# Kernel tuning notes

Hardware: AMD Instinct MI355X
Metric: run time of the kernel (lower is better)

Reference implementation:

```python
import jax, jax.numpy as jnp
import numpy as np

POINT_DIM, VOXEL_DIM, NUM_HEADS = 3, 256, 8
HEAD_DIM = VOXEL_DIM // NUM_HEADS


def _linear_params(key, fan_in, fan_out):
    kw, kb = jax.random.split(key)
    bound = 1.0 / np.sqrt(fan_in)
    W = jax.random.uniform(kw, (fan_out, fan_in), jnp.float32, -bound, bound)
    b = jax.random.uniform(kb, (fan_out,), jnp.float32, -bound, bound)
    return W, b


def setup_inputs() -> dict:
    key = jax.random.key(0)
    ks = jax.random.split(key, 7)
    points = jax.random.normal(ks[0], (2, 4096, POINT_DIM), jnp.float32)
    voxel_features = jax.random.normal(ks[1], (2, 2048, VOXEL_DIM), jnp.float32)
    Wp, bp = _linear_params(ks[2], POINT_DIM, VOXEL_DIM)
    Wq, bq = _linear_params(ks[3], VOXEL_DIM, VOXEL_DIM)
    Wk, bk = _linear_params(ks[4], VOXEL_DIM, VOXEL_DIM)
    Wv, bv = _linear_params(ks[5], VOXEL_DIM, VOXEL_DIM)
    Wf, bf = _linear_params(ks[6], VOXEL_DIM * 2, VOXEL_DIM)
    return {
        "points": points, "voxel_features": voxel_features,
        "Wp": Wp, "bp": bp, "Wq": Wq, "bq": bq,
        "Wk": Wk, "bk": bk, "Wv": Wv, "bv": bv,
        "Wf": Wf, "bf": bf,
    }


def reference(points, voxel_features, Wp, bp, Wq, bq, Wk, bk, Wv, bv, Wf, bf):
    B, N, _ = points.shape
    M = voxel_features.shape[1]
    # projections (torch Linear: x @ W.T + b)
    point_features = points @ Wp.T + bp                      # [B,N,D]
    q = (point_features @ Wq.T + bq).reshape(B, N, NUM_HEADS, HEAD_DIM)
    k = (voxel_features @ Wk.T + bk).reshape(B, M, NUM_HEADS, HEAD_DIM)
    v = (voxel_features @ Wv.T + bv).reshape(B, M, NUM_HEADS, HEAD_DIM)
    # attention scores [B,H,N,M]
    scale = 1.0 / np.sqrt(HEAD_DIM).astype(np.float32)
    attn = jnp.einsum('bnhd,bmhd->bhnm', q, k) * scale
    attn = jax.nn.softmax(attn, axis=-1)
    attended = jnp.einsum('bhnm,bmhd->bnhd', attn, v).reshape(B, N, VOXEL_DIM)
    fused = jnp.concatenate([point_features, attended], axis=-1) @ Wf.T + bf
    return fused
```

## Files before the change

### kernel.cpp

```cpp
#include <hip/hip_runtime.h>

#define B_ 2
#define N_ 4096
#define M_ 2048
#define D_ 256
#define H_ 8
#define DH_ 32
#define ROWS_ (B_*N_)
#define KVROWS_ (B_*M_)
#define PRE_ (0.17677669529663687f * 1.4426950408889634f)
#define CBASE_ 32.0f

typedef __attribute__((ext_vector_type(8))) short short8_t;
typedef __attribute__((ext_vector_type(4))) float float4_t;

#if defined(__has_builtin)
# if __has_builtin(__builtin_amdgcn_exp2f)
#  define EXP2F(x) __builtin_amdgcn_exp2f(x)
# else
#  define EXP2F(x) exp2f(x)
# endif
#else
# define EXP2F(x) exp2f(x)
#endif

__device__ __forceinline__ unsigned int rne_u(float f) {
    union { float f; unsigned int u; } c;
    c.f = f;
    return c.u + 0x7FFFu + ((c.u >> 16) & 1u);
}

__device__ __forceinline__ unsigned short f2us(float f) {
    return (unsigned short)(rne_u(f) >> 16);
}

__device__ __forceinline__ unsigned int pack2rn(float a, float b) {
    return __builtin_amdgcn_perm(rne_u(b), rne_u(a), 0x07060302u);
}

__device__ __forceinline__ unsigned int pack2tr(float a, float b) {
    union { float f; unsigned int u; } x, y;
    x.f = a; y.f = b;
    return __builtin_amdgcn_perm(y.u, x.u, 0x07060302u);
}

__device__ __forceinline__ short8_t cvt8(float4 a, float4 b) {
    union { unsigned int u[4]; short8_t s; } c;
    c.u[0] = pack2rn(a.x, a.y);
    c.u[1] = pack2rn(a.z, a.w);
    c.u[2] = pack2rn(b.x, b.y);
    c.u[3] = pack2rn(b.z, b.w);
    return c.s;
}

__device__ __forceinline__ int xcd_swz(int bid, int nwg) {
    const int cpx = nwg >> 3;
    return (bid & 7) * cpx + (bid >> 3);
}

template<int K, int NCOL, int LDSRC>
__device__ __forceinline__ void stageB2(const float* __restrict__ W, int col0, int kof,
                                        unsigned short* __restrict__ Bs, int tid)
{
    const int n = tid & (NCOL - 1), g = tid / NCOL;
    const int GROUPS = 256 / NCOL;
    const int CPT = (K / 8) / GROUPS;
    const float* src = W + (size_t)(col0 + n) * LDSRC + kof + g * (K / GROUPS);
#pragma unroll
    for (int ci = 0; ci < CPT; ci++) {
        int logc = g * CPT + ci;
        int phys = logc ^ (n & 7);
        short8_t v = cvt8(*(const float4*)(src + ci * 8), *(const float4*)(src + ci * 8 + 4));
        *(short8_t*)(Bs + (size_t)n * K + phys * 8) = v;
    }
}

template<int K>
__device__ __forceinline__ short8_t readB(const unsigned short* __restrict__ Bs,
                                          int c, int l16, int quad, int k0)
{
    int phys = ((k0 >> 3) + quad) ^ (l16 & 7);
    return *(const short8_t*)(Bs + (size_t)(16 * c + l16) * K + phys * 8);
}

__global__ __launch_bounds__(256) void g_projkv4(
    const float* __restrict__ voxel,
    const float* __restrict__ Wp, const float* __restrict__ bp,
    const float* __restrict__ Wq, const float* __restrict__ bq,
    const float* __restrict__ Wk, const float* __restrict__ bk,
    const float* __restrict__ Wv, const float* __restrict__ bv,
    const float* __restrict__ Wf, const float* __restrict__ bfb,
    unsigned short* __restrict__ k_g, unsigned short* __restrict__ vt_g,
    float* __restrict__ Wqc, float* __restrict__ Wfc)
{
    const int tid = threadIdx.x;
    const int wave = tid >> 6, lane = tid & 63, quad = lane >> 4, l16 = lane & 15;

    __shared__ unsigned short Bs[64 * 256];

    const int bid = (int)blockIdx.x;
    if (bid < 512) {
        const int lbid = xcd_swz(bid, 512);
        const int row0 = (lbid >> 3) * 64;
        const int sub  = lbid & 7;
        const int col0 = (sub >> 1) * 64;
        const bool isV = sub & 1;

        stageB2<256, 64, 256>(isV ? Wv : Wk, col0, 0, Bs, tid);

        const float* arow = voxel + (size_t)(row0 + wave * 16 + l16) * D_;
        short8_t af[8];
#pragma unroll
        for (int i = 0; i < 8; i++)
            af[i] = cvt8(*(const float4*)(arow + i * 32 + quad * 8),
                         *(const float4*)(arow + i * 32 + quad * 8 + 4));

        float4_t acc[4];
#pragma unroll
        for (int c = 0; c < 4; c++) acc[c] = (float4_t){0.f, 0.f, 0.f, 0.f};
        __syncthreads();
#pragma unroll
        for (int i = 0; i < 8; i++)
#pragma unroll
            for (int c = 0; c < 4; c++)
                acc[c] = __builtin_amdgcn_mfma_f32_16x16x32_bf16(af[i], readB<256>(Bs, c, l16, quad, i * 32), acc[c], 0, 0, 0);

        if (!isV) {
#pragma unroll
            for (int c = 0; c < 4; c++) {
                int col = col0 + 16 * c + l16;
                float bbk = bk[col];
#pragma unroll
                for (int r = 0; r < 4; r++) {
                    int row = row0 + wave * 16 + quad * 4 + r;
                    k_g[(size_t)row * D_ + col] = f2us(acc[c][r] + bbk);
                }
            }
        } else {
            const int b = row0 / M_;
            const int m0 = row0 - b * M_ + wave * 16 + quad * 4;
#pragma unroll
            for (int c = 0; c < 4; c++) {
                int col = col0 + 16 * c + l16;
                float bbv = bv[col];
                int h = col >> 5, dh = col & 31;
                unsigned int u0 = pack2rn(acc[c][0] + bbv, acc[c][1] + bbv);
                unsigned int u1 = pack2rn(acc[c][2] + bbv, acc[c][3] + bbv);
                *(uint2*)(vt_g + (size_t)((b * H_ + h) * DH_ + dh) * M_ + m0) = make_uint2(u0, u1);
            }
        }
    } else {
        const int role = bid - 512;
        float* wps = (float*)Bs;
        *(float4*)(wps + tid * 4) = make_float4(Wp[tid * 3 + 0], Wp[tid * 3 + 1],
                                                Wp[tid * 3 + 2], bp[tid]);
        __syncthreads();
        const int col = tid;
        const float* wrow = role ? (Wf + (size_t)col * 512) : (Wq + (size_t)col * 256);
        float a0 = 0.f, a1 = 0.f, a2 = 0.f, ab = 0.f;
#pragma unroll 4
        for (int d = 0; d < 256; d += 4) {
            float4 wv = *(const float4*)(wrow + d);
            float4 w0 = *(const float4*)(wps + (d + 0) * 4);
            float4 w1 = *(const float4*)(wps + (d + 1) * 4);
            float4 w2 = *(const float4*)(wps + (d + 2) * 4);
            float4 w3 = *(const float4*)(wps + (d + 3) * 4);
            a0 += wv.x * w0.x + wv.y * w1.x + wv.z * w2.x + wv.w * w3.x;
            a1 += wv.x * w0.y + wv.y * w1.y + wv.z * w2.y + wv.w * w3.y;
            a2 += wv.x * w0.z + wv.y * w1.z + wv.z * w2.z + wv.w * w3.z;
            ab += wv.x * w0.w + wv.y * w1.w + wv.z * w2.w + wv.w * w3.w;
        }
        if (role == 0) {
            *(float4*)(Wqc + (size_t)col * 4) =
                make_float4(a0 * PRE_, a1 * PRE_, a2 * PRE_, (ab + bq[col]) * PRE_);
        } else {
            *(float4*)(Wfc + (size_t)col * 4) =
                make_float4(a0, a1, a2, ab + bfb[col]);
        }
    }
}

__global__ __launch_bounds__(512) void k_attn10(
    const float* __restrict__ points, const float* __restrict__ Wqc,
    const unsigned short* __restrict__ k_g,
    const unsigned short* __restrict__ vt_g,
    unsigned short* __restrict__ att_g)
{
    const int tid = threadIdx.x;
    const int w = tid >> 6, lane = tid & 63, quad = lane >> 4, l16 = lane & 15;
    const int lbid = xcd_swz((int)blockIdx.x, B_ * H_ * (N_ / 128));
    const int nt = lbid & 31;
    const int bh = lbid >> 5;
    const int b = bh >> 3, h = bh & 7;
    const int n0 = nt * 128 + w * 16;

    __shared__ unsigned short Kt[2][64][40];
    __shared__ unsigned short Vt[2][32][72];

    const unsigned short* kbase = k_g + (size_t)(b * M_) * D_ + h * DH_;
    const unsigned short* vbase = vt_g + (size_t)(bh * DH_) * M_;

    const bool isK = (tid < 256);
    const int kr = tid >> 2, kc = tid & 3;
    const int vr = (tid - 256) >> 3, vc = tid & 7;
    const int ksr = kr ^ ((kr & 8) >> 1);

    const unsigned short* gq = isK ? (kbase + (size_t)kr * D_ + kc * 8)
                                   : (vbase + (size_t)vr * M_ + vc * 8);
    const int gstep = isK ? 64 * D_ : 64;
    unsigned short* ldst = isK ? (&Kt[0][0][0] + ksr * 40 + kc * 8)
                               : (&Vt[0][0][0] + vr * 72 + vc * 8);
    const int lstride = isK ? 2560 : 2304;

    *(short8_t*)ldst = *(const short8_t*)gq;

    const int rbas = 8 * (l16 >> 2) + (l16 & 3);
    const int rx = l16 & 4;
    int krow[4];
#pragma unroll
    for (int t = 0; t < 4; t++)
        krow[t] = (rbas + 4 * (t & 1) + 32 * (t >> 1)) ^ rx;

    const size_t qrow = (size_t)(b * N_ + n0 + l16);
    const float p0 = points[qrow * 3 + 0];
    const float p1 = points[qrow * 3 + 1];
    const float p2 = points[qrow * 3 + 2];
    float q8[8];
#pragma unroll
    for (int j = 0; j < 8; j++) {
        float4 wc = *(const float4*)(Wqc + (size_t)(h * DH_ + quad * 8 + j) * 4);
        q8[j] = p0 * wc.x + p1 * wc.y + p2 * wc.z + wc.w;
    }
    short8_t qf = cvt8(make_float4(q8[0], q8[1], q8[2], q8[3]),
                       make_float4(q8[4], q8[5], q8[6], q8[7]));

    float4_t od0 = {0.f, 0.f, 0.f, 0.f};
    float4_t od1 = {0.f, 0.f, 0.f, 0.f};
    float l_lane = 0.f;

    const float4_t zc = {-CBASE_, -CBASE_, -CBASE_, -CBASE_};

#pragma unroll 2
    for (int s = 0; s < M_ / 64; s++) {
        __syncthreads();
        const int buf = s & 1;
        const bool more = (s + 1 < M_ / 64);
        short8_t nxt;
        if (more) {
            gq += gstep;
            nxt = *(const short8_t*)gq;
        }

        float4_t st[4];
#pragma unroll
        for (int t = 0; t < 4; t++) {
            short8_t kf = *(const short8_t*)&Kt[buf][krow[t]][quad * 8];
            st[t] = __builtin_amdgcn_mfma_f32_16x16x32_bf16(kf, qf, zc, 0, 0, 0);
        }

        float psum = 0.f;
        unsigned int uu[4][2];
#pragma unroll
        for (int t = 0; t < 4; t++) {
            float p0e = EXP2F(st[t][0]);
            float p1e = EXP2F(st[t][1]);
            float p2e = EXP2F(st[t][2]);
            float p3e = EXP2F(st[t][3]);
            psum += (p0e + p1e) + (p2e + p3e);
            uu[t][0] = pack2tr(p0e, p1e);
            uu[t][1] = pack2tr(p2e, p3e);
        }
        l_lane += psum;

        union { unsigned int u[4]; short8_t s; } pa, pb2;
        pa.u[0]  = uu[0][0]; pa.u[1]  = uu[0][1]; pa.u[2]  = uu[1][0]; pa.u[3]  = uu[1][1];
        pb2.u[0] = uu[2][0]; pb2.u[1] = uu[2][1]; pb2.u[2] = uu[3][0]; pb2.u[3] = uu[3][1];

        short8_t vf00 = *(const short8_t*)&Vt[buf][l16][quad * 8];
        short8_t vf01 = *(const short8_t*)&Vt[buf][l16][32 + quad * 8];
        short8_t vf10 = *(const short8_t*)&Vt[buf][16 + l16][quad * 8];
        short8_t vf11 = *(const short8_t*)&Vt[buf][16 + l16][32 + quad * 8];
        od0 = __builtin_amdgcn_mfma_f32_16x16x32_bf16(vf00, pa.s,  od0, 0, 0, 0);
        od0 = __builtin_amdgcn_mfma_f32_16x16x32_bf16(vf01, pb2.s, od0, 0, 0, 0);
        od1 = __builtin_amdgcn_mfma_f32_16x16x32_bf16(vf10, pa.s,  od1, 0, 0, 0);
        od1 = __builtin_amdgcn_mfma_f32_16x16x32_bf16(vf11, pb2.s, od1, 0, 0, 0);

        if (more)
            *(short8_t*)(ldst + (buf ^ 1) * lstride) = nxt;
    }

    l_lane += __shfl_xor(l_lane, 16);
    l_lane += __shfl_xor(l_lane, 32);
    const float inv = 1.0f / l_lane;

    unsigned short* ob = att_g + (size_t)(b * N_ + n0 + l16) * D_ + h * DH_;
    {
        unsigned int u0 = pack2rn(od0[0] * inv, od0[1] * inv);
        unsigned int u1 = pack2rn(od0[2] * inv, od0[3] * inv);
        *(uint2*)(ob + quad * 4) = make_uint2(u0, u1);
        unsigned int u2 = pack2rn(od1[0] * inv, od1[1] * inv);
        unsigned int u3 = pack2rn(od1[2] * inv, od1[3] * inv);
        *(uint2*)(ob + 16 + quad * 4) = make_uint2(u2, u3);
    }
}

__global__ __launch_bounds__(256) void g_fuse3(
    const unsigned short* __restrict__ att_g,
    const float* __restrict__ points, const float* __restrict__ Wfc,
    const float* __restrict__ Wf,
    float* __restrict__ out)
{
    const int tid = threadIdx.x;
    const int wave = tid >> 6, lane = tid & 63, quad = lane >> 4, l16 = lane & 15;
    const int lbid = xcd_swz((int)blockIdx.x, (ROWS_ / 64) * 4);
    const int row0 = (lbid >> 2) * 64;
    const int col0 = (lbid & 3) * 64;

    __shared__ unsigned short Bs[64 * 256];

    stageB2<256, 64, 512>(Wf, col0, 256, Bs, tid);
    __syncthreads();

    float4_t acc[4];
#pragma unroll
    for (int c = 0; c < 4; c++) acc[c] = (float4_t){0.f, 0.f, 0.f, 0.f};

    const size_t arow = (size_t)(row0 + wave * 16 + l16) * D_;
#pragma unroll
    for (int k0 = 0; k0 < 256; k0 += 32) {
        short8_t af = *(const short8_t*)(att_g + arow + k0 + quad * 8);
#pragma unroll
        for (int c = 0; c < 4; c++)
            acc[c] = __builtin_amdgcn_mfma_f32_16x16x32_bf16(af, readB<256>(Bs, c, l16, quad, k0), acc[c], 0, 0, 0);
    }

    const int rbase = row0 + wave * 16 + quad * 4;
    float px[4], py[4], pz[4];
#pragma unroll
    for (int r = 0; r < 4; r++) {
        px[r] = points[(size_t)(rbase + r) * 3 + 0];
        py[r] = points[(size_t)(rbase + r) * 3 + 1];
        pz[r] = points[(size_t)(rbase + r) * 3 + 2];
    }
#pragma unroll
    for (int c = 0; c < 4; c++) {
        int col = col0 + 16 * c + l16;
        float4 wf = *(const float4*)(Wfc + (size_t)col * 4);
#pragma unroll
        for (int r = 0; r < 4; r++) {
            out[(size_t)(rbase + r) * D_ + col] =
                acc[c][r] + px[r] * wf.x + py[r] * wf.y + pz[r] * wf.z + wf.w;
        }
    }
}

extern "C" void kernel_launch(void* const* d_in, const int* in_sizes, int n_in,
                              void* d_out, int out_size, void* d_ws, size_t ws_size,
                              hipStream_t stream)
{
    const float* points = (const float*)d_in[0];
    const float* voxel  = (const float*)d_in[1];
    const float* Wp  = (const float*)d_in[2];
    const float* bp  = (const float*)d_in[3];
    const float* Wq  = (const float*)d_in[4];
    const float* bq  = (const float*)d_in[5];
    const float* Wk  = (const float*)d_in[6];
    const float* bk  = (const float*)d_in[7];
    const float* Wv  = (const float*)d_in[8];
    const float* bv  = (const float*)d_in[9];
    const float* Wf  = (const float*)d_in[10];
    const float* bfb = (const float*)d_in[11];
    float* out = (float*)d_out;

    float* Wqc = (float*)d_ws;
    float* Wfc = Wqc + 256 * 4;
    unsigned short* k_g   = (unsigned short*)(Wfc + 256 * 4);
    unsigned short* vt_g  = k_g  + (size_t)KVROWS_ * D_;
    unsigned short* att_g = vt_g + (size_t)KVROWS_ * D_;

    g_projkv4<<<dim3(514), dim3(256), 0, stream>>>(voxel, Wp, bp, Wq, bq, Wk, bk,
                                                   Wv, bv, Wf, bfb, k_g, vt_g, Wqc, Wfc);
    k_attn10<<<dim3(B_ * H_ * (N_ / 128)), dim3(512), 0, stream>>>(points, Wqc, k_g, vt_g, att_g);
    g_fuse3 <<<dim3((ROWS_ / 64) * 4), dim3(256), 0, stream>>>(att_g, points, Wfc, Wf, out);
}
```

Baseline: 133.9 us.

## Quad-buffer K/V tiles with one barrier per two steps and MFMA row sums

The attention kernel now uses four LDS buffers for the K and V tiles. It prefetches two tiles ahead and processes two 64-key steps per iteration, so there is one __syncthreads per two steps instead of one per step. The softmax denominator is now computed with an extra pair of MFMAs against a vector of bf16 ones, replacing the scalar adds and cross-lane shuffles. This doubles LDS use and adds two MFMAs per step. The row sum is now taken over bf16-rounded probabilities, which slightly changes numerics.

```diff
diff --git a/kernel.cpp b/kernel.cpp
--- a/kernel.cpp
+++ b/kernel.cpp
@@ -180,7 +180,7 @@
     }
 }
 
-__global__ __launch_bounds__(512) void k_attn10(
+__global__ __launch_bounds__(512) void k_attn11(
     const float* __restrict__ points, const float* __restrict__ Wqc,
     const unsigned short* __restrict__ k_g,
     const unsigned short* __restrict__ vt_g,
@@ -194,8 +194,8 @@
     const int b = bh >> 3, h = bh & 7;
     const int n0 = nt * 128 + w * 16;
 
-    __shared__ unsigned short Kt[2][64][40];
-    __shared__ unsigned short Vt[2][32][72];
+    __shared__ unsigned short Kt[4][64][40];
+    __shared__ unsigned short Vt[4][32][72];
 
     const unsigned short* kbase = k_g + (size_t)(b * M_) * D_ + h * DH_;
     const unsigned short* vbase = vt_g + (size_t)(bh * DH_) * M_;
@@ -205,14 +205,16 @@
     const int vr = (tid - 256) >> 3, vc = tid & 7;
     const int ksr = kr ^ ((kr & 8) >> 1);
 
+    const int gstep = isK ? 64 * D_ : 64;
     const unsigned short* gq = isK ? (kbase + (size_t)kr * D_ + kc * 8)
                                    : (vbase + (size_t)vr * M_ + vc * 8);
-    const int gstep = isK ? 64 * D_ : 64;
     unsigned short* ldst = isK ? (&Kt[0][0][0] + ksr * 40 + kc * 8)
                                : (&Vt[0][0][0] + vr * 72 + vc * 8);
     const int lstride = isK ? 2560 : 2304;
 
     *(short8_t*)ldst = *(const short8_t*)gq;
+    gq += gstep;
+    *(short8_t*)(ldst + lstride) = *(const short8_t*)gq;
 
     const int rbas = 8 * (l16 >> 2) + (l16 & 3);
     const int rx = l16 & 4;
@@ -234,64 +236,71 @@
     short8_t qf = cvt8(make_float4(q8[0], q8[1], q8[2], q8[3]),
                        make_float4(q8[4], q8[5], q8[6], q8[7]));
 
+    short8_t ones;
+#pragma unroll
+    for (int j = 0; j < 8; j++) ones[j] = (short)0x3F80;
+
     float4_t od0 = {0.f, 0.f, 0.f, 0.f};
     float4_t od1 = {0.f, 0.f, 0.f, 0.f};
-    float l_lane = 0.f;
+    float4_t lacc = {0.f, 0.f, 0.f, 0.f};
 
     const float4_t zc = {-CBASE_, -CBASE_, -CBASE_, -CBASE_};
 
+    __syncthreads();
+
+#define STEPC(KB_, VB_)                                                         \
+    do {                                                                        \
+        float4_t st[4];                                                         \
+        _Pragma("unroll")                                                       \
+        for (int t = 0; t < 4; t++) {                                           \
+            short8_t kf = *(const short8_t*)&Kt[KB_][krow[t]][quad * 8];        \
+            st[t] = __builtin_amdgcn_mfma_f32_16x16x32_bf16(kf, qf, zc, 0, 0, 0); \
+        }                                                                       \
+        unsigned int uu[4][2];                                                  \
+        _Pragma("unroll")                                                       \
+        for (int t = 0; t < 4; t++) {                                           \
+            float e0 = EXP2F(st[t][0]);                                         \
+            float e1 = EXP2F(st[t][1]);                                         \
+            float e2 = EXP2F(st[t][2]);                                         \
+            float e3 = EXP2F(st[t][3]);                                         \
+            uu[t][0] = pack2tr(e0, e1);                                         \
+            uu[t][1] = pack2tr(e2, e3);                                         \
+        }                                                                       \
+        union { unsigned int u[4]; short8_t s; } pa, pb2;                       \
+        pa.u[0]  = uu[0][0]; pa.u[1]  = uu[0][1];                               \
+        pa.u[2]  = uu[1][0]; pa.u[3]  = uu[1][1];                               \
+        pb2.u[0] = uu[2][0]; pb2.u[1] = uu[2][1];                               \
+        pb2.u[2] = uu[3][0]; pb2.u[3] = uu[3][1];                               \
+        lacc = __builtin_amdgcn_mfma_f32_16x16x32_bf16(ones, pa.s,  lacc, 0, 0, 0); \
+        lacc = __builtin_amdgcn_mfma_f32_16x16x32_bf16(ones, pb2.s, lacc, 0, 0, 0); \
+        short8_t vf00 = *(const short8_t*)&Vt[VB_][l16][quad * 8];              \
+        short8_t vf01 = *(const short8_t*)&Vt[VB_][l16][32 + quad * 8];         \
+        short8_t vf10 = *(const short8_t*)&Vt[VB_][16 + l16][quad * 8];         \
+        short8_t vf11 = *(const short8_t*)&Vt[VB_][16 + l16][32 + quad * 8];    \
+        od0 = __builtin_amdgcn_mfma_f32_16x16x32_bf16(vf00, pa.s,  od0, 0, 0, 0); \
+        od0 = __builtin_amdgcn_mfma_f32_16x16x32_bf16(vf01, pb2.s, od0, 0, 0, 0); \
+        od1 = __builtin_amdgcn_mfma_f32_16x16x32_bf16(vf10, pa.s,  od1, 0, 0, 0); \
+        od1 = __builtin_amdgcn_mfma_f32_16x16x32_bf16(vf11, pb2.s, od1, 0, 0, 0); \
+    } while (0)
+
 #pragma unroll 2
-    for (int s = 0; s < M_ / 64; s++) {
+    for (int s = 0; s < M_ / 64; s += 2) {
+        const bool m0 = (s + 2 < M_ / 64);
+        const bool m1 = (s + 3 < M_ / 64);
+        short8_t nxt0, nxt1;
+        if (m0) { gq += gstep; nxt0 = *(const short8_t*)gq; }
+        if (m1) { gq += gstep; nxt1 = *(const short8_t*)gq; }
+
+        STEPC((s) & 3, (s) & 3);
+        STEPC((s + 1) & 3, (s + 1) & 3);
+
+        if (m0) *(short8_t*)(ldst + ((s + 2) & 3) * lstride) = nxt0;
+        if (m1) *(short8_t*)(ldst + ((s + 3) & 3) * lstride) = nxt1;
         __syncthreads();
-        const int buf = s & 1;
-        const bool more = (s + 1 < M_ / 64);
-        short8_t nxt;
-        if (more) {
-            gq += gstep;
-            nxt = *(const short8_t*)gq;
-        }
-
-        float4_t st[4];
-#pragma unroll
-        for (int t = 0; t < 4; t++) {
-            short8_t kf = *(const short8_t*)&Kt[buf][krow[t]][quad * 8];
-            st[t] = __builtin_amdgcn_mfma_f32_16x16x32_bf16(kf, qf, zc, 0, 0, 0);
-        }
-
-        float psum = 0.f;
-        unsigned int uu[4][2];
-#pragma unroll
-        for (int t = 0; t < 4; t++) {
-            float p0e = EXP2F(st[t][0]);
-            float p1e = EXP2F(st[t][1]);
-            float p2e = EXP2F(st[t][2]);
-            float p3e = EXP2F(st[t][3]);
-            psum += (p0e + p1e) + (p2e + p3e);
-            uu[t][0] = pack2tr(p0e, p1e);
-            uu[t][1] = pack2tr(p2e, p3e);
-        }
-        l_lane += psum;
-
-        union { unsigned int u[4]; short8_t s; } pa, pb2;
-        pa.u[0]  = uu[0][0]; pa.u[1]  = uu[0][1]; pa.u[2]  = uu[1][0]; pa.u[3]  = uu[1][1];
-        pb2.u[0] = uu[2][0]; pb2.u[1] = uu[2][1]; pb2.u[2] = uu[3][0]; pb2.u[3] = uu[3][1];
-
-        short8_t vf00 = *(const short8_t*)&Vt[buf][l16][quad * 8];
-        short8_t vf01 = *(const short8_t*)&Vt[buf][l16][32 + quad * 8];
-        short8_t vf10 = *(const short8_t*)&Vt[buf][16 + l16][quad * 8];
-        short8_t vf11 = *(const short8_t*)&Vt[buf][16 + l16][32 + quad * 8];
-        od0 = __builtin_amdgcn_mfma_f32_16x16x32_bf16(vf00, pa.s,  od0, 0, 0, 0);
-        od0 = __builtin_amdgcn_mfma_f32_16x16x32_bf16(vf01, pb2.s, od0, 0, 0, 0);
-        od1 = __builtin_amdgcn_mfma_f32_16x16x32_bf16(vf10, pa.s,  od1, 0, 0, 0);
-        od1 = __builtin_amdgcn_mfma_f32_16x16x32_bf16(vf11, pb2.s, od1, 0, 0, 0);
-
-        if (more)
-            *(short8_t*)(ldst + (buf ^ 1) * lstride) = nxt;
-    }
-
-    l_lane += __shfl_xor(l_lane, 16);
-    l_lane += __shfl_xor(l_lane, 32);
-    const float inv = 1.0f / l_lane;
+    }
+#undef STEPC
+
+    const float inv = 1.0f / lacc[0];
 
     unsigned short* ob = att_g + (size_t)(b * N_ + n0 + l16) * D_ + h * DH_;
     {
@@ -380,6 +389,6 @@
 
     g_projkv4<<<dim3(514), dim3(256), 0, stream>>>(voxel, Wp, bp, Wq, bq, Wk, bk,
                                                    Wv, bv, Wf, bfb, k_g, vt_g, Wqc, Wfc);
-    k_attn10<<<dim3(B_ * H_ * (N_ / 128)), dim3(512), 0, stream>>>(points, Wqc, k_g, vt_g, att_g);
+    k_attn11<<<dim3(B_ * H_ * (N_ / 128)), dim3(512), 0, stream>>>(points, Wqc, k_g, vt_g, att_g);
     g_fuse3 <<<dim3((ROWS_ / 64) * 4), dim3(256), 0, stream>>>(att_g, points, Wfc, Wf, out);
 }
```

Result: no change. 132.1 us, median of 3 (-1.3%).
